# Kernel tuning notes

Hardware: AMD Instinct MI355X
Metric: run time of the kernel (lower is better)

The kernel has to match this reference:

```python
import jax, jax.numpy as jnp
import numpy as np

B, N, DIN, DOUT = 8, 2048, 512, 512

def setup_inputs() -> dict:
    key = jax.random.key(0)
    kx, ka, kw, kb, kattn = jax.random.split(key, 5)
    x = jax.random.normal(kx, (B, N, DIN), dtype=jnp.float32)
    adjacency_matrix = jax.random.randint(ka, (B, N, N), 0, 2, dtype=jnp.int32)
    # nn.Linear(in,out): weight [out,in], bias [out]
    lim_w = float(np.sqrt(1.0 / DIN))
    W = jax.random.uniform(kw, (DOUT, DIN), minval=-lim_w, maxval=lim_w, dtype=jnp.float32)
    b = jax.random.uniform(kb, (DOUT,), minval=-lim_w, maxval=lim_w, dtype=jnp.float32)
    # xavier_uniform for attn [out,out]
    lim_a = float(np.sqrt(6.0 / (DOUT + DOUT)))
    attn = jax.random.uniform(kattn, (DOUT, DOUT), minval=-lim_a, maxval=lim_a, dtype=jnp.float32)
    return {"x": x, "adjacency_matrix": adjacency_matrix, "W": W, "b": b, "attn": attn}

def reference(x, adjacency_matrix, W, b, attn):
    h = jnp.einsum('bni,oi->bno', x, W) + b                 # [B,N,DOUT]
    ha = jnp.einsum('bmi,ij->bmj', h, attn)                  # h @ attn
    scores = jnp.einsum('bmj,bnj->bmn', ha, h)               # bilinear pairwise scores
    scores = jnp.where(adjacency_matrix == 0, -jnp.inf, scores)
    attn_weights = jax.nn.softmax(scores, axis=-1)           # adjacency-masked softmax
    x_out = jnp.einsum('bmn,bnd->bmd', attn_weights, h)      # weighted aggregation
    return jax.nn.elu(x_out)
```

## Files before the change

kernel.cpp:

```cpp
#include <hip/hip_runtime.h>
#include <cstdint>
#include <cstddef>

typedef unsigned short u16;
using f16x8 = __attribute__((ext_vector_type(8))) _Float16;
using f32x4 = __attribute__((ext_vector_type(4))) float;
using u16x4 = __attribute__((ext_vector_type(4))) unsigned short;

__device__ __forceinline__ u16 f2h(float f) {
  union { _Float16 h; u16 u; } c;
  c.h = (_Float16)f;
  return c.u;
}

__device__ __forceinline__ void gl_lds16(const void* g, void* lds) {
  __builtin_amdgcn_global_load_lds(
      (const __attribute__((address_space(1))) void*)(uintptr_t)g,
      (__attribute__((address_space(3))) void*)(uint32_t)(uintptr_t)lds,
      16, 0, 0);
}

template <int N> __device__ __forceinline__ void vmcnt_wait() {
  if constexpr (N == 0)      asm volatile("s_waitcnt vmcnt(0)" ::: "memory");
  else if constexpr (N == 3) asm volatile("s_waitcnt vmcnt(3)" ::: "memory");
  else if constexpr (N == 4) asm volatile("s_waitcnt vmcnt(4)" ::: "memory");
  else static_assert(N == 0, "unsupported vmcnt literal");
}

__device__ __forceinline__ void block_sync() {
  asm volatile("" ::: "memory");
  __builtin_amdgcn_s_barrier();
  asm volatile("" ::: "memory");
}

template <int ROWS>
__device__ __forceinline__ void stage32(const u16* g, int ldk, u16* lds, int t) {
#pragma unroll
  for (int i = 0; i < ROWS / 128; ++i) {
    const int s   = i * 512 + t;
    const int row = s >> 2;
    const int gc  = (s & 3) ^ ((s >> 3) & 3);
    gl_lds16(g + (size_t)row * ldk + gc * 8,
             lds + (size_t)(i * 512 + (t & ~63)) * 8);
  }
}

template <int NF>
__device__ __forceinline__ void compute_tile32(
    const u16* pA, const u16* pB, f32x4 (&acc)[8][NF],
    int wm, int wn, int lm, int cq)
{
  f16x8 bf[NF];
#pragma unroll
  for (int nf = 0; nf < NF; ++nf)
    bf[nf] = *(const f16x8*)(pB + (wn + nf * 16 + lm) * 32 + cq * 8);
#pragma unroll
  for (int mf = 0; mf < 8; ++mf) {
    f16x8 a0 = *(const f16x8*)(pA + (wm + mf * 16 + lm) * 32 + cq * 8);
#pragma unroll
    for (int nf = 0; nf < NF; ++nf)
      acc[mf][nf] = __builtin_amdgcn_mfma_f32_16x16x32_f16(a0, bf[nf], acc[mf][nf], 0, 0, 0);
  }
}

template <int BN, int MODE>
__global__ __launch_bounds__(512, 2) void gemm32(
    const u16* __restrict__ A, const u16* __restrict__ Bt,
    void* __restrict__ Cv, const float* __restrict__ bias,
    int M, int Ncols, int K,
    long long strideA, long long strideB, long long strideC)
{
  constexpr int NF  = BN / 64;
  constexpr int LPT = 2 + BN / 128;

  __shared__ __align__(16) u16 sA0[256 * 32];
  __shared__ __align__(16) u16 sA1[256 * 32];
  __shared__ __align__(16) u16 sA2[256 * 32];
  __shared__ __align__(16) u16 sA3[256 * 32];
  __shared__ __align__(16) u16 sB0[BN * 32];
  __shared__ __align__(16) u16 sB1[BN * 32];
  __shared__ __align__(16) u16 sB2[BN * 32];
  __shared__ __align__(16) u16 sB3[BN * 32];

  const int bz = blockIdx.z;
  A  += (size_t)bz * strideA;
  Bt += (size_t)bz * strideB;

  const int m0 = blockIdx.y * 256;
  const int n0 = blockIdx.x * BN;
  const int t    = threadIdx.x;
  const int lane = t & 63;
  const int wave = t >> 6;
  const int wm   = (wave >> 2) * 128;
  const int wn   = (wave & 3) * (BN / 4);
  const int lm   = lane & 15;
  const int quad = lane >> 4;
  const int cq   = quad ^ ((lm >> 1) & 3);

  f32x4 acc[8][NF];
#pragma unroll
  for (int i = 0; i < 8; ++i)
#pragma unroll
    for (int j = 0; j < NF; ++j) acc[i][j] = f32x4{0.f, 0.f, 0.f, 0.f};

  const u16* Ag = A + (size_t)m0 * K;
  const u16* Bg = Bt + (size_t)n0 * K;

  const int nk = K >> 5;

  stage32<256>(Ag,      K, sA0, t);  stage32<BN>(Bg,      K, sB0, t);
  stage32<256>(Ag + 32, K, sA1, t);  stage32<BN>(Bg + 32, K, sB1, t);

  for (int kt = 0; kt < nk - 4; kt += 4) {
    vmcnt_wait<LPT>(); block_sync();
    stage32<256>(Ag + (size_t)(kt + 2) * 32, K, sA2, t);
    stage32<BN >(Bg + (size_t)(kt + 2) * 32, K, sB2, t);
    compute_tile32<NF>(sA0, sB0, acc, wm, wn, lm, cq);

    vmcnt_wait<LPT>(); block_sync();
    stage32<256>(Ag + (size_t)(kt + 3) * 32, K, sA3, t);
    stage32<BN >(Bg + (size_t)(kt + 3) * 32, K, sB3, t);
    compute_tile32<NF>(sA1, sB1, acc, wm, wn, lm, cq);

    vmcnt_wait<LPT>(); block_sync();
    stage32<256>(Ag + (size_t)(kt + 4) * 32, K, sA0, t);
    stage32<BN >(Bg + (size_t)(kt + 4) * 32, K, sB0, t);
    compute_tile32<NF>(sA2, sB2, acc, wm, wn, lm, cq);

    vmcnt_wait<LPT>(); block_sync();
    stage32<256>(Ag + (size_t)(kt + 5) * 32, K, sA1, t);
    stage32<BN >(Bg + (size_t)(kt + 5) * 32, K, sB1, t);
    compute_tile32<NF>(sA3, sB3, acc, wm, wn, lm, cq);
  }

  vmcnt_wait<LPT>(); block_sync();
  stage32<256>(Ag + (size_t)(nk - 2) * 32, K, sA2, t);
  stage32<BN >(Bg + (size_t)(nk - 2) * 32, K, sB2, t);
  compute_tile32<NF>(sA0, sB0, acc, wm, wn, lm, cq);

  vmcnt_wait<LPT>(); block_sync();
  stage32<256>(Ag + (size_t)(nk - 1) * 32, K, sA3, t);
  stage32<BN >(Bg + (size_t)(nk - 1) * 32, K, sB3, t);
  compute_tile32<NF>(sA1, sB1, acc, wm, wn, lm, cq);

  vmcnt_wait<LPT>(); block_sync();
  compute_tile32<NF>(sA2, sB2, acc, wm, wn, lm, cq);

  vmcnt_wait<0>(); block_sync();
  compute_tile32<NF>(sA3, sB3, acc, wm, wn, lm, cq);

  if (MODE == 0) {
    u16* C = (u16*)Cv + (size_t)bz * strideC;
#pragma unroll
    for (int nf = 0; nf < NF; ++nf) {
      const int col = n0 + wn + nf * 16 + lm;
      const float bv = bias ? bias[col] : 0.f;
#pragma unroll
      for (int mf = 0; mf < 8; ++mf)
#pragma unroll
        for (int r = 0; r < 4; ++r) {
          const int row = m0 + wm + mf * 16 + quad * 4 + r;
          C[(size_t)row * Ncols + col] = f2h(acc[mf][nf][r] + bv);
        }
    }
  } else {
    float* C = (float*)Cv + (size_t)bz * strideC;
#pragma unroll
    for (int nf = 0; nf < NF; ++nf) {
      const int col = n0 + wn + nf * 16 + lm;
#pragma unroll
      for (int mf = 0; mf < 8; ++mf)
#pragma unroll
        for (int r = 0; r < 4; ++r) {
          const int row = m0 + wm + mf * 16 + quad * 4 + r;
          C[(size_t)row * Ncols + col] = acc[mf][nf][r];
        }
    }
  }
}

__global__ __launch_bounds__(512, 2) void fused_attn(
    const u16* __restrict__ Qg, const u16* __restrict__ Kg,
    const u16* __restrict__ Vt, const int* __restrict__ adj,
    float* __restrict__ out)
{
  constexpr int N = 2048, D = 512;
  __shared__ __align__(16) u16 sK[64 * 512];
  __shared__ __align__(16) u16 sP[64 * 64];
  __shared__ float sm[64], sl[64], sf[64];
  __shared__ float pmx[2][64], psm[2][64];

  const int bz = blockIdx.y;
  const int q0 = blockIdx.x * 64;
  const u16* Qb = Qg + ((size_t)bz * N + q0) * D;
  const u16* Kb = Kg + (size_t)bz * N * D;
  const u16* Vb = Vt + (size_t)bz * D * N;
  const int* Ab = adj + ((size_t)bz * N + q0) * N;
  float*     Ob = out + ((size_t)bz * N + q0) * D;

  const int t = threadIdx.x;
  const int lane = t & 63, wave = t >> 6;
  const int lm = lane & 15, quad = lane >> 4;
  const int qf  = wave >> 1;
  const int kf0 = (wave & 1) * 2;

  f16x8 qreg[16];
#pragma unroll
  for (int s = 0; s < 16; ++s)
    qreg[s] = *(const f16x8*)(Qb + (size_t)(qf * 16 + lm) * D + s * 32 + quad * 8);

  if (t < 64) { sm[t] = -1e30f; sl[t] = 0.f; }

  f32x4 o_acc[4][4];
#pragma unroll
  for (int i = 0; i < 4; ++i)
#pragma unroll
    for (int j = 0; j < 4; ++j) o_acc[i][j] = f32x4{0.f, 0.f, 0.f, 0.f};

  __syncthreads();

  for (int kv = 0; kv < N; kv += 64) {
#pragma unroll
    for (int i = 0; i < 8; ++i) {
      const int s = i * 512 + t;
      const int row = s >> 6, c = s & 63;
      gl_lds16(Kb + (size_t)(kv + row) * D + (size_t)((c ^ (row & 7)) * 8),
               sK + (size_t)(i * 512 + (t & ~63)) * 8);
    }
    int am[2][4];
#pragma unroll
    for (int j = 0; j < 2; ++j)
#pragma unroll
      for (int r = 0; r < 4; ++r)
        am[j][r] = Ab[(size_t)(qf * 16 + quad * 4 + r) * N + kv + (kf0 + j) * 16 + lm];
    f16x8 vf[4][2];
#pragma unroll
    for (int df = 0; df < 4; ++df)
#pragma unroll
      for (int ks = 0; ks < 2; ++ks)
        vf[df][ks] = *(const f16x8*)(Vb + (size_t)(wave * 64 + df * 16 + lm) * N
                                        + kv + ks * 32 + quad * 8);

    __syncthreads();

    f32x4 sfr[2];
    sfr[0] = f32x4{0.f, 0.f, 0.f, 0.f};
    sfr[1] = f32x4{0.f, 0.f, 0.f, 0.f};
#pragma unroll
    for (int j = 0; j < 2; ++j) {
      const int krow = (kf0 + j) * 16 + lm;
#pragma unroll
      for (int s = 0; s < 16; ++s) {
        f16x8 kfr = *(const f16x8*)(sK + (size_t)krow * 512
                                       + (size_t)((((s * 4 + quad) ^ (lm & 7)) * 8)));
        sfr[j] = __builtin_amdgcn_mfma_f32_16x16x32_f16(qreg[s], kfr, sfr[j], 0, 0, 0);
      }
    }
    float vmax[4];
#pragma unroll
    for (int r = 0; r < 4; ++r) {
      sfr[0][r] = am[0][r] ? sfr[0][r] : -1e30f;
      sfr[1][r] = am[1][r] ? sfr[1][r] : -1e30f;
      vmax[r] = fmaxf(sfr[0][r], sfr[1][r]);
    }
#pragma unroll
    for (int r = 0; r < 4; ++r)
#pragma unroll
      for (int o = 1; o < 16; o <<= 1) vmax[r] = fmaxf(vmax[r], __shfl_xor(vmax[r], o));
    if (lm == 0)
#pragma unroll
      for (int r = 0; r < 4; ++r) pmx[wave & 1][qf * 16 + quad * 4 + r] = vmax[r];
    __syncthreads();

    if (t < 64) {
      const float mo = sm[t];
      const float mn = fmaxf(mo, fmaxf(pmx[0][t], pmx[1][t]));
      sm[t] = mn;
      sf[t] = __expf(mo - mn);
    }
    __syncthreads();

    float vsum[4];
#pragma unroll
    for (int r = 0; r < 4; ++r) {
      const int row = qf * 16 + quad * 4 + r;
      const float mn = sm[row];
      const float e0 = __expf(sfr[0][r] - mn);
      const float e1 = __expf(sfr[1][r] - mn);
      vsum[r] = e0 + e1;
      const int rq = row & 7;
      sP[(size_t)row * 64 + (size_t)((((kf0    ) * 2 + (lm >> 3)) ^ rq) * 8) + (lm & 7)] = f2h(e0);
      sP[(size_t)row * 64 + (size_t)((((kf0 + 1) * 2 + (lm >> 3)) ^ rq) * 8) + (lm & 7)] = f2h(e1);
    }
#pragma unroll
    for (int r = 0; r < 4; ++r)
#pragma unroll
      for (int o = 1; o < 16; o <<= 1) vsum[r] += __shfl_xor(vsum[r], o);
    if (lm == 0)
#pragma unroll
      for (int r = 0; r < 4; ++r) psm[wave & 1][qf * 16 + quad * 4 + r] = vsum[r];
    __syncthreads();

    if (t < 64) sl[t] = sl[t] * sf[t] + psm[0][t] + psm[1][t];

#pragma unroll
    for (int qi = 0; qi < 4; ++qi) {
      float fr[4];
#pragma unroll
      for (int r = 0; r < 4; ++r) fr[r] = sf[qi * 16 + quad * 4 + r];
#pragma unroll
      for (int df = 0; df < 4; ++df)
#pragma unroll
        for (int r = 0; r < 4; ++r) o_acc[qi][df][r] *= fr[r];
#pragma unroll
      for (int ks = 0; ks < 2; ++ks) {
        const int prow = qi * 16 + lm;
        f16x8 pa = *(const f16x8*)(sP + (size_t)prow * 64
                                      + (size_t)((((ks * 4 + quad) ^ (lm & 7)) * 8)));
#pragma unroll
        for (int df = 0; df < 4; ++df)
          o_acc[qi][df] = __builtin_amdgcn_mfma_f32_16x16x32_f16(pa, vf[df][ks], o_acc[qi][df], 0, 0, 0);
      }
    }
    __syncthreads();
  }

#pragma unroll
  for (int qi = 0; qi < 4; ++qi) {
    float il[4];
#pragma unroll
    for (int r = 0; r < 4; ++r) il[r] = 1.f / sl[qi * 16 + quad * 4 + r];
#pragma unroll
    for (int df = 0; df < 4; ++df)
#pragma unroll
      for (int r = 0; r < 4; ++r) {
        float v = o_acc[qi][df][r] * il[r];
        v = v > 0.f ? v : expm1f(v);
        Ob[(size_t)(qi * 16 + quad * 4 + r) * D + wave * 64 + df * 16 + lm] = v;
      }
  }
}

__global__ __launch_bounds__(256) void transpose_u16(
    const u16* __restrict__ in, u16* __restrict__ outp, int R, int C)
{
  __shared__ u16 tile[64][65];
  const size_t base = (size_t)blockIdx.z * R * C;
  const int r0 = blockIdx.y * 64, c0 = blockIdx.x * 64;
  const int t = threadIdx.x;
  const int c = t & 63, rr = t >> 6;
#pragma unroll
  for (int i = 0; i < 16; ++i) {
    const int r = rr + i * 4;
    tile[r][c] = in[base + (size_t)(r0 + r) * C + c0 + c];
  }
  __syncthreads();
  const int rp = t & 63, cc = t >> 6;
#pragma unroll
  for (int i = 0; i < 16; ++i) {
    const int cq2 = cc + i * 4;
    outp[base + (size_t)(c0 + cq2) * R + r0 + rp] = tile[rp][cq2];
  }
}

__global__ __launch_bounds__(256) void cvt_f32_f16(
    const float* __restrict__ in, u16* __restrict__ outp, int n4)
{
  const int i = blockIdx.x * 256 + threadIdx.x;
  if (i >= n4) return;
  float4 v = ((const float4*)in)[i];
  u16x4 o; o[0] = f2h(v.x); o[1] = f2h(v.y); o[2] = f2h(v.z); o[3] = f2h(v.w);
  ((u16x4*)outp)[i] = o;
}

__global__ __launch_bounds__(256) void transpose_cvt(
    const float* __restrict__ in, u16* __restrict__ outp, int R, int C)
{
  const int idx = blockIdx.x * 256 + threadIdx.x;
  const int i = idx / C, j = idx % C;
  outp[(size_t)j * R + i] = f2h(in[idx]);
}

extern "C" void kernel_launch(void* const* d_in, const int* in_sizes, int n_in,
                              void* d_out, int out_size, void* d_ws, size_t ws_size,
                              hipStream_t stream) {
  (void)in_sizes; (void)n_in; (void)out_size;
  const float* x    = (const float*)d_in[0];
  const int*   adj  = (const int*)d_in[1];
  const float* W    = (const float*)d_in[2];
  const float* bvec = (const float*)d_in[3];
  const float* attn = (const float*)d_in[4];
  float* out = (float*)d_out;

  constexpr int B = 8, N = 2048, D = 512;
  constexpr size_t MN = (size_t)B * N;

  char* ws = (char*)d_ws;
  size_t off = 0;
  auto take = [&](size_t bytes) -> char* {
    char* p = ws + off;
    off += (bytes + 255) & ~(size_t)255;
    return p;
  };
  u16* xh   = (u16*)take(MN * D * 2);
  u16* Wh   = (u16*)take((size_t)D * D * 2);
  u16* attT = (u16*)take((size_t)D * D * 2);
  u16* h    = (u16*)take(MN * D * 2);
  u16* hT   = (u16*)take(MN * D * 2);
  u16* ha   = (u16*)take(MN * D * 2);
  if (ws_size < off) return;

  cvt_f32_f16<<<dim3((unsigned)(MN * D / 4 / 256)), 256, 0, stream>>>(x, xh, (int)(MN * D / 4));
  cvt_f32_f16<<<dim3(D * D / 4 / 256), 256, 0, stream>>>(W, Wh, D * D / 4);
  transpose_cvt<<<dim3(D * D / 256), 256, 0, stream>>>(attn, attT, D, D);

  gemm32<128, 0><<<dim3(D / 128, MN / 256, 1), 512, 0, stream>>>(
      xh, Wh, h, bvec, (int)MN, D, D, 0, 0, 0);
  transpose_u16<<<dim3(D / 64, N / 64, B), 256, 0, stream>>>(h, hT, N, D);
  gemm32<128, 0><<<dim3(D / 128, MN / 256, 1), 512, 0, stream>>>(
      h, attT, ha, nullptr, (int)MN, D, D, 0, 0, 0);

  fused_attn<<<dim3(N / 64, B), 512, 0, stream>>>(ha, h, hT, adj, out);
}
```

Before: 515.4 us.

## Double-buffer K tiles in LDS and keep softmax running stats in registers

K tiles are now staged into two LDS buffers, and the next tile is prefetched with global_load_lds while the current one feeds the MFMAs. This removes the barrier that used to wait for each K load. Running max and sum now live in per-thread registers, which drops the single-thread update phases and two block barriers per iteration. The cost is doubled K staging in LDS (about 136KB per block), which likely allows only one 512-thread block per CU instead of the two the launch bounds target. That lower occupancy could offset the overlap gain.

Result: slower. 660.7 us (+28.2%).

```diff
diff --git a/kernel.cpp b/kernel.cpp
--- a/kernel.cpp
+++ b/kernel.cpp
@@ -31,6 +31,12 @@
   asm volatile("" ::: "memory");
   __builtin_amdgcn_s_barrier();
   asm volatile("" ::: "memory");
+}
+
+__device__ __forceinline__ void lds_sync() {
+  asm volatile("s_waitcnt lgkmcnt(0)" ::: "memory");
+  __builtin_amdgcn_s_barrier();
+  __builtin_amdgcn_sched_barrier(0);
 }
 
 template <int ROWS>
@@ -185,9 +191,10 @@
     float* __restrict__ out)
 {
   constexpr int N = 2048, D = 512;
-  __shared__ __align__(16) u16 sK[64 * 512];
+  __shared__ __align__(16) u16 sK0[64 * 512];
+  __shared__ __align__(16) u16 sK1[64 * 512];
   __shared__ __align__(16) u16 sP[64 * 64];
-  __shared__ float sm[64], sl[64], sf[64];
+  __shared__ float sf[64], sl[64];
   __shared__ float pmx[2][64], psm[2][64];
 
   const int bz = blockIdx.y;
@@ -202,14 +209,17 @@
   const int lane = t & 63, wave = t >> 6;
   const int lm = lane & 15, quad = lane >> 4;
   const int qf  = wave >> 1;
-  const int kf0 = (wave & 1) * 2;
+  const int kh  = wave & 1;
+  const int kf0 = kh * 2;
 
   f16x8 qreg[16];
 #pragma unroll
   for (int s = 0; s < 16; ++s)
     qreg[s] = *(const f16x8*)(Qb + (size_t)(qf * 16 + lm) * D + s * 32 + quad * 8);
 
-  if (t < 64) { sm[t] = -1e30f; sl[t] = 0.f; }
+  float m_reg[4], l_reg[4];
+#pragma unroll
+  for (int r = 0; r < 4; ++r) { m_reg[r] = -1e30f; l_reg[r] = 0.f; }
 
   f32x4 o_acc[4][4];
 #pragma unroll
@@ -217,16 +227,21 @@
 #pragma unroll
     for (int j = 0; j < 4; ++j) o_acc[i][j] = f32x4{0.f, 0.f, 0.f, 0.f};
 
-  __syncthreads();
-
-  for (int kv = 0; kv < N; kv += 64) {
+  auto stageK = [&](u16* lds, int kv) {
 #pragma unroll
     for (int i = 0; i < 8; ++i) {
       const int s = i * 512 + t;
       const int row = s >> 6, c = s & 63;
       gl_lds16(Kb + (size_t)(kv + row) * D + (size_t)((c ^ (row & 7)) * 8),
-               sK + (size_t)(i * 512 + (t & ~63)) * 8);
-    }
+               lds + (size_t)(i * 512 + (t & ~63)) * 8);
+    }
+  };
+
+  stageK(sK0, 0);
+  __syncthreads();
+
+  auto body = [&](const u16* curK, u16* nxtK, int T) {
+    const int kv = T * 64;
     int am[2][4];
 #pragma unroll
     for (int j = 0; j < 2; ++j)
@@ -240,8 +255,7 @@
       for (int ks = 0; ks < 2; ++ks)
         vf[df][ks] = *(const f16x8*)(Vb + (size_t)(wave * 64 + df * 16 + lm) * N
                                         + kv + ks * 32 + quad * 8);
-
-    __syncthreads();
+    if (T + 1 < 32) stageK(nxtK, kv + 64);
 
     f32x4 sfr[2];
     sfr[0] = f32x4{0.f, 0.f, 0.f, 0.f};
@@ -251,8 +265,8 @@
       const int krow = (kf0 + j) * 16 + lm;
 #pragma unroll
       for (int s = 0; s < 16; ++s) {
-        f16x8 kfr = *(const f16x8*)(sK + (size_t)krow * 512
-                                       + (size_t)((((s * 4 + quad) ^ (lm & 7)) * 8)));
+        f16x8 kfr = *(const f16x8*)(curK + (size_t)krow * 512
+                                        + (size_t)((((s * 4 + quad) ^ (lm & 7)) * 8)));
         sfr[j] = __builtin_amdgcn_mfma_f32_16x16x32_f16(qreg[s], kfr, sfr[j], 0, 0, 0);
       }
     }
@@ -269,22 +283,16 @@
       for (int o = 1; o < 16; o <<= 1) vmax[r] = fmaxf(vmax[r], __shfl_xor(vmax[r], o));
     if (lm == 0)
 #pragma unroll
-      for (int r = 0; r < 4; ++r) pmx[wave & 1][qf * 16 + quad * 4 + r] = vmax[r];
-    __syncthreads();
-
-    if (t < 64) {
-      const float mo = sm[t];
-      const float mn = fmaxf(mo, fmaxf(pmx[0][t], pmx[1][t]));
-      sm[t] = mn;
-      sf[t] = __expf(mo - mn);
-    }
-    __syncthreads();
-
-    float vsum[4];
+      for (int r = 0; r < 4; ++r) pmx[kh][qf * 16 + quad * 4 + r] = vmax[r];
+    lds_sync();
+
+    float f_[4], vsum[4];
 #pragma unroll
     for (int r = 0; r < 4; ++r) {
       const int row = qf * 16 + quad * 4 + r;
-      const float mn = sm[row];
+      const float mn = fmaxf(m_reg[r], fmaxf(pmx[0][row], pmx[1][row]));
+      f_[r] = __expf(m_reg[r] - mn);
+      m_reg[r] = mn;
       const float e0 = __expf(sfr[0][r] - mn);
       const float e1 = __expf(sfr[1][r] - mn);
       vsum[r] = e0 + e1;
@@ -298,10 +306,17 @@
       for (int o = 1; o < 16; o <<= 1) vsum[r] += __shfl_xor(vsum[r], o);
     if (lm == 0)
 #pragma unroll
-      for (int r = 0; r < 4; ++r) psm[wave & 1][qf * 16 + quad * 4 + r] = vsum[r];
-    __syncthreads();
-
-    if (t < 64) sl[t] = sl[t] * sf[t] + psm[0][t] + psm[1][t];
+      for (int r = 0; r < 4; ++r) psm[kh][qf * 16 + quad * 4 + r] = vsum[r];
+    if (kh == 0 && lm == 0)
+#pragma unroll
+      for (int r = 0; r < 4; ++r) sf[qf * 16 + quad * 4 + r] = f_[r];
+    lds_sync();
+
+#pragma unroll
+    for (int r = 0; r < 4; ++r) {
+      const int row = qf * 16 + quad * 4 + r;
+      l_reg[r] = l_reg[r] * f_[r] + psm[0][row] + psm[1][row];
+    }
 
 #pragma unroll
     for (int qi = 0; qi < 4; ++qi) {
@@ -323,7 +338,17 @@
       }
     }
     __syncthreads();
-  }
+  };
+
+  for (int kt = 0; kt < 32; kt += 2) {
+    body(sK0, sK1, kt);
+    body(sK1, sK0, kt + 1);
+  }
+
+  if (kh == 0 && lm == 0)
+#pragma unroll
+    for (int r = 0; r < 4; ++r) sl[qf * 16 + quad * 4 + r] = l_reg[r];
+  __syncthreads();
 
 #pragma unroll
   for (int qi = 0; qi < 4; ++qi) {
```

## Unfuse attention: compute scores via batched GEMM, then masked softmax-PV kernel

Applied to the files above, without the earlier changes.

Splits the fused flash-style attention kernel into a batched GEMM that writes the full fp32 score matrix to workspace, followed by a new kernel that streams scores and adjacency, runs an online masked softmax and multiplies by V. The new kernel uses 32-row query blocks, double-buffered shared arrays, per-thread running max and sum, and one fewer barrier per tile. The intent is to replace the low-occupancy QK^T inner loop with a high-efficiency GEMM tile. The cost is writing and rereading 128 MB of scores, plus a per-batch fallback loop when workspace is small.

Measured after the change: 537.6 us. 4.3% more time.

```diff
diff --git a/kernel.cpp b/kernel.cpp
--- a/kernel.cpp
+++ b/kernel.cpp
@@ -179,60 +179,50 @@
   }
 }
 
-__global__ __launch_bounds__(512, 2) void fused_attn(
-    const u16* __restrict__ Qg, const u16* __restrict__ Kg,
-    const u16* __restrict__ Vt, const int* __restrict__ adj,
-    float* __restrict__ out)
+__global__ __launch_bounds__(512, 4) void smpv(
+    const float* __restrict__ S, const int* __restrict__ adj,
+    const u16* __restrict__ Vt, float* __restrict__ out)
 {
   constexpr int N = 2048, D = 512;
-  __shared__ __align__(16) u16 sK[64 * 512];
-  __shared__ __align__(16) u16 sP[64 * 64];
-  __shared__ float sm[64], sl[64], sf[64];
-  __shared__ float pmx[2][64], psm[2][64];
+  __shared__ __align__(16) u16 sP[2][32 * 64];
+  __shared__ float sf[2][32];
+  __shared__ float pmx[2][4][32], psm[2][4][32];
+  __shared__ float sl[32];
 
   const int bz = blockIdx.y;
-  const int q0 = blockIdx.x * 64;
-  const u16* Qb = Qg + ((size_t)bz * N + q0) * D;
-  const u16* Kb = Kg + (size_t)bz * N * D;
-  const u16* Vb = Vt + (size_t)bz * D * N;
-  const int* Ab = adj + ((size_t)bz * N + q0) * N;
-  float*     Ob = out + ((size_t)bz * N + q0) * D;
+  const int q0 = blockIdx.x * 32;
+  const float* Sb = S   + ((size_t)bz * N + q0) * N;
+  const int*   Ab = adj + ((size_t)bz * N + q0) * N;
+  const u16*   Vb = Vt  + (size_t)bz * D * N;
+  float*       Ob = out + ((size_t)bz * N + q0) * D;
 
   const int t = threadIdx.x;
   const int lane = t & 63, wave = t >> 6;
   const int lm = lane & 15, quad = lane >> 4;
-  const int qf  = wave >> 1;
-  const int kf0 = (wave & 1) * 2;
-
-  f16x8 qreg[16];
-#pragma unroll
-  for (int s = 0; s < 16; ++s)
-    qreg[s] = *(const f16x8*)(Qb + (size_t)(qf * 16 + lm) * D + s * 32 + quad * 8);
-
-  if (t < 64) { sm[t] = -1e30f; sl[t] = 0.f; }
-
-  f32x4 o_acc[4][4];
-#pragma unroll
-  for (int i = 0; i < 4; ++i)
+  const int qf = wave >> 2;
+  const int kf = wave & 3;
+
+  float m_reg[4], l_reg[4];
+#pragma unroll
+  for (int r = 0; r < 4; ++r) { m_reg[r] = -1e30f; l_reg[r] = 0.f; }
+
+  f32x4 o_acc[2][4];
+#pragma unroll
+  for (int i = 0; i < 2; ++i)
 #pragma unroll
     for (int j = 0; j < 4; ++j) o_acc[i][j] = f32x4{0.f, 0.f, 0.f, 0.f};
 
-  __syncthreads();
-
-  for (int kv = 0; kv < N; kv += 64) {
-#pragma unroll
-    for (int i = 0; i < 8; ++i) {
-      const int s = i * 512 + t;
-      const int row = s >> 6, c = s & 63;
-      gl_lds16(Kb + (size_t)(kv + row) * D + (size_t)((c ^ (row & 7)) * 8),
-               sK + (size_t)(i * 512 + (t & ~63)) * 8);
-    }
-    int am[2][4];
-#pragma unroll
-    for (int j = 0; j < 2; ++j)
-#pragma unroll
-      for (int r = 0; r < 4; ++r)
-        am[j][r] = Ab[(size_t)(qf * 16 + quad * 4 + r) * N + kv + (kf0 + j) * 16 + lm];
+  for (int T = 0; T < 32; ++T) {
+    const int kv = T * 64, tp = T & 1;
+    const int col = kv + kf * 16 + lm;
+
+    float sv[4]; int am[4];
+#pragma unroll
+    for (int r = 0; r < 4; ++r) {
+      const int row = qf * 16 + quad * 4 + r;
+      sv[r] = Sb[(size_t)row * N + col];
+      am[r] = Ab[(size_t)row * N + col];
+    }
     f16x8 vf[4][2];
 #pragma unroll
     for (int df = 0; df < 4; ++df)
@@ -241,56 +231,30 @@
         vf[df][ks] = *(const f16x8*)(Vb + (size_t)(wave * 64 + df * 16 + lm) * N
                                         + kv + ks * 32 + quad * 8);
 
-    __syncthreads();
-
-    f32x4 sfr[2];
-    sfr[0] = f32x4{0.f, 0.f, 0.f, 0.f};
-    sfr[1] = f32x4{0.f, 0.f, 0.f, 0.f};
-#pragma unroll
-    for (int j = 0; j < 2; ++j) {
-      const int krow = (kf0 + j) * 16 + lm;
-#pragma unroll
-      for (int s = 0; s < 16; ++s) {
-        f16x8 kfr = *(const f16x8*)(sK + (size_t)krow * 512
-                                       + (size_t)((((s * 4 + quad) ^ (lm & 7)) * 8)));
-        sfr[j] = __builtin_amdgcn_mfma_f32_16x16x32_f16(qreg[s], kfr, sfr[j], 0, 0, 0);
-      }
-    }
     float vmax[4];
 #pragma unroll
-    for (int r = 0; r < 4; ++r) {
-      sfr[0][r] = am[0][r] ? sfr[0][r] : -1e30f;
-      sfr[1][r] = am[1][r] ? sfr[1][r] : -1e30f;
-      vmax[r] = fmaxf(sfr[0][r], sfr[1][r]);
-    }
+    for (int r = 0; r < 4; ++r) { sv[r] = am[r] ? sv[r] : -1e30f; vmax[r] = sv[r]; }
 #pragma unroll
     for (int r = 0; r < 4; ++r)
 #pragma unroll
       for (int o = 1; o < 16; o <<= 1) vmax[r] = fmaxf(vmax[r], __shfl_xor(vmax[r], o));
     if (lm == 0)
 #pragma unroll
-      for (int r = 0; r < 4; ++r) pmx[wave & 1][qf * 16 + quad * 4 + r] = vmax[r];
+      for (int r = 0; r < 4; ++r) pmx[tp][kf][qf * 16 + quad * 4 + r] = vmax[r];
     __syncthreads();
 
-    if (t < 64) {
-      const float mo = sm[t];
-      const float mn = fmaxf(mo, fmaxf(pmx[0][t], pmx[1][t]));
-      sm[t] = mn;
-      sf[t] = __expf(mo - mn);
-    }
-    __syncthreads();
-
-    float vsum[4];
+    float f_[4], vsum[4];
 #pragma unroll
     for (int r = 0; r < 4; ++r) {
       const int row = qf * 16 + quad * 4 + r;
-      const float mn = sm[row];
-      const float e0 = __expf(sfr[0][r] - mn);
-      const float e1 = __expf(sfr[1][r] - mn);
-      vsum[r] = e0 + e1;
-      const int rq = row & 7;
-      sP[(size_t)row * 64 + (size_t)((((kf0    ) * 2 + (lm >> 3)) ^ rq) * 8) + (lm & 7)] = f2h(e0);
-      sP[(size_t)row * 64 + (size_t)((((kf0 + 1) * 2 + (lm >> 3)) ^ rq) * 8) + (lm & 7)] = f2h(e1);
+      float mn = fmaxf(fmaxf(pmx[tp][0][row], pmx[tp][1][row]),
+                       fmaxf(pmx[tp][2][row], pmx[tp][3][row]));
+      mn = fmaxf(m_reg[r], mn);
+      f_[r] = __expf(m_reg[r] - mn);
+      m_reg[r] = mn;
+      const float e = __expf(sv[r] - mn);
+      vsum[r] = e;
+      sP[tp][row * 64 + (((kf * 2 + (lm >> 3)) ^ (row & 7)) * 8) + (lm & 7)] = f2h(e);
     }
 #pragma unroll
     for (int r = 0; r < 4; ++r)
@@ -298,16 +262,24 @@
       for (int o = 1; o < 16; o <<= 1) vsum[r] += __shfl_xor(vsum[r], o);
     if (lm == 0)
 #pragma unroll
-      for (int r = 0; r < 4; ++r) psm[wave & 1][qf * 16 + quad * 4 + r] = vsum[r];
+      for (int r = 0; r < 4; ++r) psm[tp][kf][qf * 16 + quad * 4 + r] = vsum[r];
+    if (kf == 0 && lm == 0)
+#pragma unroll
+      for (int r = 0; r < 4; ++r) sf[tp][qf * 16 + quad * 4 + r] = f_[r];
     __syncthreads();
 
-    if (t < 64) sl[t] = sl[t] * sf[t] + psm[0][t] + psm[1][t];
-
-#pragma unroll
-    for (int qi = 0; qi < 4; ++qi) {
+#pragma unroll
+    for (int r = 0; r < 4; ++r) {
+      const int row = qf * 16 + quad * 4 + r;
+      l_reg[r] = l_reg[r] * f_[r]
+               + psm[tp][0][row] + psm[tp][1][row] + psm[tp][2][row] + psm[tp][3][row];
+    }
+
+#pragma unroll
+    for (int qi = 0; qi < 2; ++qi) {
       float fr[4];
 #pragma unroll
-      for (int r = 0; r < 4; ++r) fr[r] = sf[qi * 16 + quad * 4 + r];
+      for (int r = 0; r < 4; ++r) fr[r] = sf[tp][qi * 16 + quad * 4 + r];
 #pragma unroll
       for (int df = 0; df < 4; ++df)
 #pragma unroll
@@ -315,18 +287,22 @@
 #pragma unroll
       for (int ks = 0; ks < 2; ++ks) {
         const int prow = qi * 16 + lm;
-        f16x8 pa = *(const f16x8*)(sP + (size_t)prow * 64
-                                      + (size_t)((((ks * 4 + quad) ^ (lm & 7)) * 8)));
+        f16x8 pa = *(const f16x8*)(sP[tp] + prow * 64
+                                    + (((ks * 4 + quad) ^ (prow & 7)) * 8));
 #pragma unroll
         for (int df = 0; df < 4; ++df)
           o_acc[qi][df] = __builtin_amdgcn_mfma_f32_16x16x32_f16(pa, vf[df][ks], o_acc[qi][df], 0, 0, 0);
       }
     }
-    __syncthreads();
-  }
-
-#pragma unroll
-  for (int qi = 0; qi < 4; ++qi) {
+  }
+
+  if (kf == 0 && lm == 0)
+#pragma unroll
+    for (int r = 0; r < 4; ++r) sl[qf * 16 + quad * 4 + r] = l_reg[r];
+  __syncthreads();
+
+#pragma unroll
+  for (int qi = 0; qi < 2; ++qi) {
     float il[4];
 #pragma unroll
     for (int r = 0; r < 4; ++r) il[r] = 1.f / sl[qi * 16 + quad * 4 + r];
@@ -408,7 +384,13 @@
   u16* h    = (u16*)take(MN * D * 2);
   u16* hT   = (u16*)take(MN * D * 2);
   u16* ha   = (u16*)take(MN * D * 2);
-  if (ws_size < off) return;
+
+  auto al = [](size_t b) { return (b + 255) & ~(size_t)255; };
+  const size_t szSf = al((size_t)B * N * N * 4);
+  const size_t szSb = al((size_t)N * N * 4);
+  const bool full  = ws_size >= off + szSf;
+  const bool ok_pb = ws_size >= off + szSb;
+  if (!full && !ok_pb) return;
 
   cvt_f32_f16<<<dim3((unsigned)(MN * D / 4 / 256)), 256, 0, stream>>>(x, xh, (int)(MN * D / 4));
   cvt_f32_f16<<<dim3(D * D / 4 / 256), 256, 0, stream>>>(W, Wh, D * D / 4);
@@ -420,5 +402,19 @@
   gemm32<128, 0><<<dim3(D / 128, MN / 256, 1), 512, 0, stream>>>(
       h, attT, ha, nullptr, (int)MN, D, D, 0, 0, 0);
 
-  fused_attn<<<dim3(N / 64, B), 512, 0, stream>>>(ha, h, hT, adj, out);
-}
+  if (full) {
+    float* S = (float*)take(szSf);
+    gemm32<256, 1><<<dim3(N / 256, N / 256, B), 512, 0, stream>>>(
+        ha, h, S, nullptr, N, N, D,
+        (long long)N * D, (long long)N * D, (long long)N * N);
+    smpv<<<dim3(N / 32, B), 512, 0, stream>>>(S, adj, hT, out);
+  } else {
+    float* S = (float*)take(szSb);
+    for (int b = 0; b < B; ++b) {
+      gemm32<256, 1><<<dim3(N / 256, N / 256, 1), 512, 0, stream>>>(
+          ha + (size_t)b * N * D, h + (size_t)b * N * D, S, nullptr, N, N, D, 0, 0, 0);
+      smpv<<<dim3(N / 32, 1), 512, 0, stream>>>(S, adj + (size_t)b * N * N, hT + (size_t)b * D * N,
+                                                out + (size_t)b * N * D);
+    }
+  }
+}
```
